# Kernel optimization log

Hardware: AMD Instinct MI355X
Metric: run time of the kernel (lower is better)

Reference implementation:

```python
import jax, jax.numpy as jnp
import numpy as np

E = 1024   # embed_dim
H = 16     # num_heads
D = E // H # head dim = 64
NUM_BUCKETS = 32
MAX_DISTANCE = 128


def _relative_position_bucket(rel, num_buckets=NUM_BUCKETS, max_distance=MAX_DISTANCE):
    # T5-style bucketing (bidirectional): sign half + log-spaced far buckets.
    nb = num_buckets // 2
    buckets = (rel > 0).astype(jnp.int32) * nb
    rel = jnp.abs(rel)
    max_exact = nb // 2
    is_small = rel < max_exact
    # clamp to >=1 before log to avoid -inf on the masked-out branch
    rel_f = jnp.maximum(rel, 1).astype(jnp.float32)
    large = max_exact + (
        jnp.log(rel_f / max_exact) / np.log(max_distance / max_exact) * (nb - max_exact)
    ).astype(jnp.int32)
    large = jnp.minimum(large, nb - 1)
    return buckets + jnp.where(is_small, rel, large)


def setup_inputs() -> dict:
    key = jax.random.key(0)
    ks = jax.random.split(key, 6)
    B, S, K = 2, 2048, 2048
    w = 0.02
    return {
        "hidden_states": jax.random.normal(ks[0], (B, S, E), jnp.float32),
        "key_value_states": jax.random.normal(ks[1], (B, K, E), jnp.float32),
        "Wq": jax.random.normal(ks[2], (E, E), jnp.float32) * w,
        "Wkv": jax.random.normal(ks[3], (E, 2 * E), jnp.float32) * w,
        "Wo": jax.random.normal(ks[4], (E, E), jnp.float32) * w,
        "rel_bias": jax.random.normal(ks[5], (NUM_BUCKETS, H), jnp.float32) * w,
    }


def reference(hidden_states, key_value_states, Wq, Wkv, Wo, rel_bias):
    B, S, _ = hidden_states.shape
    K = key_value_states.shape[1]
    # projections (no bias, no 1/sqrt(d) scaling — T5 style)
    q = (hidden_states @ Wq).reshape(B, S, H, D).transpose(0, 2, 1, 3)      # [B,H,S,D]
    kv = (key_value_states @ Wkv).reshape(B, K, 2, H, D)
    k = kv[:, :, 0].transpose(0, 2, 1, 3)                                   # [B,H,K,D]
    v = kv[:, :, 1].transpose(0, 2, 1, 3)                                   # [B,H,K,D]
    scores = jnp.einsum('bhsd,bhkd->bhsk', q, k)                            # [B,H,S,K]
    # relative position bias
    rel = jnp.arange(K)[None, :] - jnp.arange(S)[:, None]                   # [S,K]
    buckets = _relative_position_bucket(rel)                                # [S,K]
    bias = rel_bias[buckets].transpose(2, 0, 1)[None]                       # [1,H,S,K]
    scores = scores + bias
    attn = jax.nn.softmax(scores.astype(jnp.float32), axis=-1).astype(scores.dtype)
    out = jnp.einsum('bhsk,bhkd->bshd', attn, v).reshape(B, S, E)
    return out @ Wo
```

## Files before the change

kernel.cpp:

```cpp
#include <hip/hip_runtime.h>
#include <hip/hip_bf16.h>
#include <math.h>

typedef __hip_bfloat16 bf16;
typedef __bf16 bf16x4 __attribute__((ext_vector_type(4)));
typedef __bf16 bf16x8 __attribute__((ext_vector_type(8)));
typedef float f32x4 __attribute__((ext_vector_type(4)));
typedef float f32x16 __attribute__((ext_vector_type(16)));
typedef unsigned short us4 __attribute__((ext_vector_type(4)));

#define LOG2E 1.44269504088896340736f

#if defined(__has_builtin)
#if __has_builtin(__builtin_amdgcn_exp2f)
#define EXP2(x) __builtin_amdgcn_exp2f(x)
#else
#define EXP2(x) exp2f(x)
#endif
#else
#define EXP2(x) exp2f(x)
#endif


__device__ inline __bf16 f2b(float f) {
  __hip_bfloat16 h = __float2bfloat16(f);
  return *reinterpret_cast<__bf16*>(&h);
}
__device__ inline unsigned short b2u(float f) {
  __hip_bfloat16 h = __float2bfloat16(f);
  return *reinterpret_cast<unsigned short*>(&h);
}
__device__ inline unsigned short b2u_fast(float f) {
  union { float f; unsigned u; } v;
  v.f = f;
  return (unsigned short)((v.u + 0x8000u) >> 16);
}
__device__ inline bf16x8 ld16(const bf16* p) {
  bf16x4 lo = *(const bf16x4*)p;
  bf16x4 hi = *(const bf16x4*)(p + 4);
  return __builtin_shufflevector(lo, hi, 0, 1, 2, 3, 4, 5, 6, 7);
}
__device__ inline void st16(bf16* p, uint4 v) {
  *(uint2*)p = make_uint2(v.x, v.y);
  *(uint2*)(p + 4) = make_uint2(v.z, v.w);
}
__device__ inline us4 shfl32_us4(us4 v) {
  uint2 u = *(uint2*)&v;
  u.x = __shfl_xor(u.x, 32);
  u.y = __shfl_xor(u.y, 32);
  return *(us4*)&u;
}
__device__ inline bf16x8 mk8(us4 lo, us4 hi) {
  bf16x4 l = *(bf16x4*)&lo;
  bf16x4 h = *(bf16x4*)&hi;
  return __builtin_shufflevector(l, h, 0, 1, 2, 3, 4, 5, 6, 7);
}
__device__ inline void async16(const bf16* g, bf16* l) {
  __builtin_amdgcn_global_load_lds(
      (const __attribute__((address_space(1))) unsigned int*)g,
      (__attribute__((address_space(3))) unsigned int*)l, 16, 0, 0);
}

__global__ void cast2_k(const float* __restrict__ a, const float* __restrict__ b,
                        bf16* __restrict__ oa, bf16* __restrict__ ob) {
  int gid = blockIdx.x * 256 + threadIdx.x;
  const float* in = (gid < 524288) ? a : b;
  bf16* out = (gid < 524288) ? oa : ob;
  int i = (gid & 524287) * 8;
  float4 a0 = *(const float4*)(in + i);
  float4 a1 = *(const float4*)(in + i + 4);
  bf16x8 v;
  v[0] = f2b(a0.x); v[1] = f2b(a0.y); v[2] = f2b(a0.z); v[3] = f2b(a0.w);
  v[4] = f2b(a1.x); v[5] = f2b(a1.y); v[6] = f2b(a1.z); v[7] = f2b(a1.w);
  *(bf16x8*)(out + i) = v;
}

__global__ void prep_k(const float* __restrict__ Wq, const float* __restrict__ Wkv,
                       const float* __restrict__ Wo, const float* __restrict__ rel_bias,
                       bf16* __restrict__ WqT, bf16* __restrict__ WkvT,
                       bf16* __restrict__ WoT, float* __restrict__ lut) {
  __shared__ float tile[32][33];
  int z = blockIdx.z;
  int tx = threadIdx.x, ty = threadIdx.y;
  if (z == 3) {
    if (blockIdx.y != 0 || blockIdx.x >= 16) return;
    int r = blockIdx.x * 256 + ty * 32 + tx;
    int rel = r - 2048;
    int bkt = rel > 0 ? 16 : 0;
    int ar = rel < 0 ? -rel : rel;
    int idx;
    if (ar < 8) {
      idx = bkt + ar;
    } else {
      double t = log((double)ar / 8.0) / log(16.0) * 8.0;
      int lg = 8 + (int)t;
      if (lg > 15) lg = 15;
      idx = bkt + lg;
    }
    for (int h = 0; h < 16; ++h)
      lut[h * 4096 + r] = rel_bias[idx * 16 + h] * LOG2E;
    return;
  }
  const float* in = z == 0 ? Wq : (z == 1 ? Wkv : Wo);
  bf16* out = z == 0 ? WqT : (z == 1 ? WkvT : WoT);
  int cols = z == 1 ? 2048 : 1024;
  int c0 = blockIdx.x * 32;
  if (c0 >= cols) return;
  int r0 = blockIdx.y * 32;
  for (int i = ty; i < 32; i += 8)
    tile[i][tx] = in[(size_t)(r0 + i) * cols + c0 + tx];
  __syncthreads();
  for (int i = ty; i < 32; i += 8)
    out[(size_t)(c0 + i) * 1024 + r0 + tx] = __float2bfloat16(tile[tx][i]);
}

__global__ __launch_bounds__(256) void gemm_qkv_k(const bf16* __restrict__ hbf,
                                                  const bf16* __restrict__ kbf,
                                                  const bf16* __restrict__ WqT,
                                                  const bf16* __restrict__ WkvT,
                                                  bf16* __restrict__ Qb,
                                                  bf16* __restrict__ Kb,
                                                  bf16* __restrict__ Vt) {
  __shared__ __align__(16) bf16 As[128 * 32];
  __shared__ __align__(16) bf16 Bs[128 * 32];
  const int tid = threadIdx.x;
  const int lane = tid & 63;
  const int w = tid >> 6;
  const int wm = (w >> 1) * 64;
  const int wn = (w & 1) * 64;
  const int l15 = lane & 15;
  const int quad = lane >> 4;
  const int srow = lane >> 2;
  const int skg = lane & 3;

  const bool isQ = blockIdx.y < 8;
  const bf16* A = isQ ? hbf : kbf;
  const bf16* Bt = isQ ? WqT : WkvT;
  const int n0 = (isQ ? blockIdx.y : blockIdx.y - 8) * 128;
  const int m0 = blockIdx.x * 128;
  const bool isV = (!isQ) && (n0 >= 1024);

  f32x4 acc[4][4];
#pragma unroll
  for (int i = 0; i < 4; ++i)
#pragma unroll
    for (int j = 0; j < 4; ++j) acc[i][j] = (f32x4){0.f, 0.f, 0.f, 0.f};

  for (int k0 = 0; k0 < 1024; k0 += 32) {
    __syncthreads();
#pragma unroll
    for (int rep = 0; rep < 2; ++rep) {
      int seg = w * 2 + rep;
      async16(A + (size_t)(m0 + seg * 16 + srow) * 1024 + k0 + skg * 8, As + seg * 512);
      async16(Bt + (size_t)(n0 + seg * 16 + srow) * 1024 + k0 + skg * 8, Bs + seg * 512);
    }
    __syncthreads();
    bf16x8 af[4], bfr[4];
#pragma unroll
    for (int i = 0; i < 4; ++i)
      af[i] = *(const bf16x8*)(As + (wm + i * 16 + l15) * 32 + quad * 8);
#pragma unroll
    for (int j = 0; j < 4; ++j)
      bfr[j] = *(const bf16x8*)(Bs + (wn + j * 16 + l15) * 32 + quad * 8);
    if (isV) {
#pragma unroll
      for (int i = 0; i < 4; ++i)
#pragma unroll
        for (int j = 0; j < 4; ++j)
          acc[i][j] = __builtin_amdgcn_mfma_f32_16x16x32_bf16(af[i], bfr[j], acc[i][j], 0, 0, 0);
    } else {
#pragma unroll
      for (int i = 0; i < 4; ++i)
#pragma unroll
        for (int j = 0; j < 4; ++j)
          acc[i][j] = __builtin_amdgcn_mfma_f32_16x16x32_bf16(bfr[j], af[i], acc[i][j], 0, 0, 0);
    }
  }

  if (isV) {
#pragma unroll
    for (int i = 0; i < 4; ++i) {
      int gmb = m0 + wm + i * 16 + quad * 4;
      int b = gmb >> 11, kp = gmb & 2047;
#pragma unroll
      for (int j = 0; j < 4; ++j) {
        int gn = n0 + wn + j * 16 + l15;
        int h = (gn >> 6) & 15, d = gn & 63;
        us4 pk;
#pragma unroll
        for (int r = 0; r < 4; ++r) pk[r] = b2u(acc[i][j][r]);
        *(us4*)(Vt + ((((size_t)b * 16 + h) * 64 + d) << 11) + kp) = pk;
      }
    }
    return;
  }
  const float scale = isQ ? LOG2E : 1.0f;
  bf16* dst = isQ ? Qb : Kb;
#pragma unroll
  for (int i = 0; i < 4; ++i) {
    int gm = m0 + wm + i * 16 + l15;
    int b = gm >> 11, s = gm & 2047;
#pragma unroll
    for (int j = 0; j < 4; ++j) {
      int gn = n0 + wn + j * 16 + quad * 4;
      int h = (gn >> 6) & 15, d0 = gn & 63;
      us4 pk;
#pragma unroll
      for (int r = 0; r < 4; ++r) pk[r] = b2u(acc[i][j][r] * scale);
      *(us4*)(dst + ((((size_t)b * 16 + h) * 2048 + s) << 6) + d0) = pk;
    }
  }
}

__global__ __launch_bounds__(256) void gemm_o_k(const bf16* __restrict__ A,
                                                const bf16* __restrict__ Bt,
                                                float* __restrict__ C0) {
  __shared__ __align__(16) bf16 As[128 * 32];
  __shared__ __align__(16) bf16 Bs[64 * 32];
  const int tid = threadIdx.x;
  const int lane = tid & 63;
  const int w = tid >> 6;
  const int wm = w * 32;
  const int m0 = blockIdx.x * 128;
  const int n0 = blockIdx.y * 64;
  const int l15 = lane & 15;
  const int quad = lane >> 4;
  const int srow = lane >> 2;
  const int skg = lane & 3;

  f32x4 acc[2][4];
#pragma unroll
  for (int i = 0; i < 2; ++i)
#pragma unroll
    for (int j = 0; j < 4; ++j) acc[i][j] = (f32x4){0.f, 0.f, 0.f, 0.f};

  for (int k0 = 0; k0 < 1024; k0 += 32) {
    __syncthreads();
#pragma unroll
    for (int rep = 0; rep < 2; ++rep) {
      int seg = w * 2 + rep;
      async16(A + (size_t)(m0 + seg * 16 + srow) * 1024 + k0 + skg * 8, As + seg * 512);
    }
    async16(Bt + (size_t)(n0 + w * 16 + srow) * 1024 + k0 + skg * 8, Bs + w * 512);
    __syncthreads();
    bf16x8 af[2], bfr[4];
#pragma unroll
    for (int i = 0; i < 2; ++i)
      af[i] = *(const bf16x8*)(As + (wm + i * 16 + l15) * 32 + quad * 8);
#pragma unroll
    for (int j = 0; j < 4; ++j)
      bfr[j] = *(const bf16x8*)(Bs + (j * 16 + l15) * 32 + quad * 8);
#pragma unroll
    for (int i = 0; i < 2; ++i)
#pragma unroll
      for (int j = 0; j < 4; ++j)
        acc[i][j] = __builtin_amdgcn_mfma_f32_16x16x32_bf16(bfr[j], af[i], acc[i][j], 0, 0, 0);
  }
#pragma unroll
  for (int i = 0; i < 2; ++i) {
    int gm = m0 + wm + i * 16 + l15;
#pragma unroll
    for (int j = 0; j < 4; ++j) {
      int gn = n0 + j * 16 + quad * 4;
      *(f32x4*)(C0 + (size_t)gm * 1024 + gn) = acc[i][j];
    }
  }
}

#define STK 68
#define SVK 136
#define KS_OFF 8704
#define VS_OFF 43520
__global__ __launch_bounds__(512, 2) void attn_k(const bf16* __restrict__ Qb,
                                                 const bf16* __restrict__ Kb,
                                                 const bf16* __restrict__ Vt,
                                                 const float* __restrict__ lut,
                                                 bf16* __restrict__ Ob) {
  __shared__ __align__(16) char smem[78336];
  float* lbias = (float*)smem;
  bf16* Ksb = (bf16*)(smem + KS_OFF);
  bf16* Vsb = (bf16*)(smem + VS_OFF);

  const int tid = threadIdx.x;
  const int lane = tid & 63;
  const int w = tid >> 6;
  const int wq = w & 3;
  const int kg = w >> 2;
  const int t256 = tid & 255;
  const int q31 = lane & 31;
  const int half = lane >> 5;

  bf16* Ks = Ksb + kg * (128 * STK);
  bf16* Vs = Vsb + kg * (64 * SVK);

  const int qt = blockIdx.x;
  const int bh = blockIdx.y;
  const int h = bh & 15, b = bh >> 4;
  const int qb = qt * 128;

  const int gbase = h * 4096 + 1921 - qb;
  for (int t = tid; t < 2175; t += 512) lbias[t] = lut[gbase + t];

  const size_t base = (size_t)bh * 2048 * 64;
  const size_t vbase = (size_t)bh * 64 * 2048;
  const int qg = qb + wq * 32 + q31;

  bf16x8 qf[4];
#pragma unroll
  for (int c = 0; c < 4; ++c)
    qf[c] = *(const bf16x8*)(Qb + base + (size_t)qg * 64 + c * 16 + half * 8);

  f32x16 oacc[2];
#pragma unroll
  for (int dj = 0; dj < 2; ++dj)
#pragma unroll
    for (int r = 0; r < 16; ++r) oacc[dj][r] = 0.f;
  float l_run = 0.f;

  const int kt0 = kg * 128;

  uint4 kr[4], vr[4];
#pragma unroll
  for (int rep = 0; rep < 4; ++rep) {
    int slot = t256 + rep * 256;
    kr[rep] = *(const uint4*)(Kb + base + (size_t)(kt0 + (slot >> 3)) * 64 + (slot & 7) * 8);
    vr[rep] = *(const uint4*)(Vt + vbase + (size_t)(slot >> 4) * 2048 + kt0 + (slot & 15) * 8);
  }

  for (int it = 0; it < 8; ++it) {
    const int kt = it * 256 + kt0;
    __syncthreads();
#pragma unroll
    for (int rep = 0; rep < 4; ++rep) {
      int slot = t256 + rep * 256;
      st16(Ks + (slot >> 3) * STK + (slot & 7) * 8, kr[rep]);
      st16(Vs + (slot >> 4) * SVK + (slot & 15) * 8, vr[rep]);
    }
    __syncthreads();
    if (it < 7) {
      const int nkt = kt + 256;
#pragma unroll
      for (int rep = 0; rep < 4; ++rep) {
        int slot = t256 + rep * 256;
        kr[rep] = *(const uint4*)(Kb + base + (size_t)(nkt + (slot >> 3)) * 64 + (slot & 7) * 8);
        vr[rep] = *(const uint4*)(Vt + vbase + (size_t)(slot >> 4) * 2048 + nkt + (slot & 15) * 8);
      }
    }

    const int xbase = kt + 127 + 4 * half - wq * 32 - q31;
#pragma unroll
    for (int mt = 0; mt < 4; ++mt) {
      f32x16 sacc;
#pragma unroll
      for (int a2 = 0; a2 < 4; ++a2)
#pragma unroll
        for (int rr = 0; rr < 4; ++rr)
          sacc[4 * a2 + rr] = lbias[xbase + mt * 32 + 8 * a2 + rr];
#pragma unroll
      for (int c = 0; c < 4; ++c) {
        bf16x8 kf = ld16(Ks + (mt * 32 + q31) * STK + c * 16 + half * 8);
        sacc = __builtin_amdgcn_mfma_f32_32x32x16_bf16(kf, qf[c], sacc, 0, 0, 0);
      }

      us4 ownq[4];
      f32x4 sv = (f32x4){0.f, 0.f, 0.f, 0.f};
#pragma unroll
      for (int a = 0; a < 4; ++a) {
        us4 pk;
#pragma unroll
        for (int rr = 0; rr < 4; ++rr) {
          float p = EXP2(sacc[4 * a + rr]);
          sv[rr] += p;
          pk[rr] = b2u_fast(p);
        }
        ownq[a] = pk;
      }
      l_run += (sv[0] + sv[1]) + (sv[2] + sv[3]);

      us4 rcv0 = shfl32_us4(half ? ownq[0] : ownq[1]);
      us4 rcv1 = shfl32_us4(half ? ownq[2] : ownq[3]);

#pragma unroll
      for (int p = 0; p < 2; ++p) {
        us4 rc = p ? rcv1 : rcv0;
        bf16x8 pfc = half ? mk8(rc, ownq[2 * p + 1]) : mk8(ownq[2 * p], rc);
#pragma unroll
        for (int dj = 0; dj < 2; ++dj) {
          bf16x8 vf = ld16(Vs + (dj * 32 + q31) * SVK + (mt * 2 + p) * 16 + half * 8);
          oacc[dj] = __builtin_amdgcn_mfma_f32_32x32x16_bf16(vf, pfc, oacc[dj], 0, 0, 0);
        }
      }
    }
  }

  l_run += __shfl_xor(l_run, 32);

  __syncthreads();
  float* mbuf = (float*)smem;
  if (kg) {
    float* p = mbuf + ((size_t)(wq * 64 + lane)) * 35;
    p[0] = l_run;
#pragma unroll
    for (int dj = 0; dj < 2; ++dj)
#pragma unroll
      for (int r = 0; r < 16; ++r) p[1 + dj * 16 + r] = oacc[dj][r];
  }
  __syncthreads();
  if (kg) return;

  const float* p = mbuf + ((size_t)(wq * 64 + lane)) * 35;
  float inv = 1.0f / (l_run + p[0]);

#pragma unroll
  for (int dj = 0; dj < 2; ++dj)
#pragma unroll
    for (int g = 0; g < 4; ++g) {
      us4 pk;
#pragma unroll
      for (int rr = 0; rr < 4; ++rr)
        pk[rr] = b2u((oacc[dj][4 * g + rr] + p[1 + dj * 16 + 4 * g + rr]) * inv);
      int d0 = dj * 32 + 8 * g + 4 * half;
      *(us4*)(Ob + ((size_t)(b * 2048 + qg)) * 1024 + h * 64 + d0) = pk;
    }
}

extern "C" void kernel_launch(void* const* d_in, const int* in_sizes, int n_in,
                              void* d_out, int out_size, void* d_ws, size_t ws_size,
                              hipStream_t stream) {
  const float* hidden = (const float*)d_in[0];
  const float* kvs    = (const float*)d_in[1];
  const float* Wq     = (const float*)d_in[2];
  const float* Wkv    = (const float*)d_in[3];
  const float* Wo     = (const float*)d_in[4];
  const float* relb   = (const float*)d_in[5];
  float* out = (float*)d_out;

  char* ws = (char*)d_ws;
  bf16* WqT  = (bf16*)(ws + (size_t)0);
  bf16* WkvT = (bf16*)(ws + ((size_t)2 << 20));
  bf16* WoT  = (bf16*)(ws + ((size_t)6 << 20));
  bf16* Ob   = (bf16*)(ws + ((size_t)8 << 20));
  bf16* hbf  = Ob;
  bf16* Qb   = (bf16*)(ws + ((size_t)16 << 20));
  bf16* Kb   = (bf16*)(ws + ((size_t)24 << 20));
  bf16* Vt   = (bf16*)(ws + ((size_t)32 << 20));
  float* LUT = (float*)(ws + ((size_t)40 << 20));
  bf16* kbf  = (bf16*)d_out;

  prep_k<<<dim3(64, 32, 4), dim3(32, 8), 0, stream>>>(Wq, Wkv, Wo, relb, WqT, WkvT, WoT, LUT);
  cast2_k<<<4096, 256, 0, stream>>>(hidden, kvs, hbf, kbf);
  gemm_qkv_k<<<dim3(32, 24), 256, 0, stream>>>(hbf, kbf, WqT, WkvT, Qb, Kb, Vt);
  attn_k<<<dim3(16, 32), 512, 0, stream>>>(Qb, Kb, Vt, LUT, Ob);
  gemm_o_k<<<dim3(32, 16), 256, 0, stream>>>(Ob, WoT, out);
}
```

Measured before the change: 226.9 us.

## Remap attention blocks so each XCD owns whole heads; drop K/V register prefetch

The attention grid becomes 1D. Block ids are remapped so all 16 query tiles of a given batch-head land on the same XCD (blocks are assigned to XCDs round-robin), which should let that XCD's L2 reuse the K/V tiles. The register-staged prefetch of the next K/V tile is also removed: each tile is now loaded and stored to shared memory in the same iteration. This cuts register pressure and may raise occupancy, but load latency is no longer hidden behind compute.

After: 218.8 us (median of 2 runs). 3.6% less time.

```diff
diff --git a/kernel.cpp b/kernel.cpp
--- a/kernel.cpp
+++ b/kernel.cpp
@@ -293,8 +293,11 @@
   bf16* Ks = Ksb + kg * (128 * STK);
   bf16* Vs = Vsb + kg * (64 * SVK);
 
-  const int qt = blockIdx.x;
-  const int bh = blockIdx.y;
+  const int wg = blockIdx.x;
+  const int xcd = wg & 7;
+  const int slot = wg >> 3;
+  const int bh = xcd * 4 + (slot >> 4);
+  const int qt = slot & 15;
   const int h = bh & 15, b = bh >> 4;
   const int qb = qt * 128;
 
@@ -319,33 +322,25 @@
 
   const int kt0 = kg * 128;
 
-  uint4 kr[4], vr[4];
-#pragma unroll
-  for (int rep = 0; rep < 4; ++rep) {
-    int slot = t256 + rep * 256;
-    kr[rep] = *(const uint4*)(Kb + base + (size_t)(kt0 + (slot >> 3)) * 64 + (slot & 7) * 8);
-    vr[rep] = *(const uint4*)(Vt + vbase + (size_t)(slot >> 4) * 2048 + kt0 + (slot & 15) * 8);
-  }
-
   for (int it = 0; it < 8; ++it) {
     const int kt = it * 256 + kt0;
     __syncthreads();
-#pragma unroll
-    for (int rep = 0; rep < 4; ++rep) {
-      int slot = t256 + rep * 256;
-      st16(Ks + (slot >> 3) * STK + (slot & 7) * 8, kr[rep]);
-      st16(Vs + (slot >> 4) * SVK + (slot & 15) * 8, vr[rep]);
-    }
-    __syncthreads();
-    if (it < 7) {
-      const int nkt = kt + 256;
+    {
+      uint4 kr[4], vr[4];
 #pragma unroll
       for (int rep = 0; rep < 4; ++rep) {
-        int slot = t256 + rep * 256;
-        kr[rep] = *(const uint4*)(Kb + base + (size_t)(nkt + (slot >> 3)) * 64 + (slot & 7) * 8);
-        vr[rep] = *(const uint4*)(Vt + vbase + (size_t)(slot >> 4) * 2048 + nkt + (slot & 15) * 8);
-      }
-    }
+        int slot2 = t256 + rep * 256;
+        kr[rep] = *(const uint4*)(Kb + base + (size_t)(kt + (slot2 >> 3)) * 64 + (slot2 & 7) * 8);
+        vr[rep] = *(const uint4*)(Vt + vbase + (size_t)(slot2 >> 4) * 2048 + kt + (slot2 & 15) * 8);
+      }
+#pragma unroll
+      for (int rep = 0; rep < 4; ++rep) {
+        int slot2 = t256 + rep * 256;
+        st16(Ks + (slot2 >> 3) * STK + (slot2 & 7) * 8, kr[rep]);
+        st16(Vs + (slot2 >> 4) * SVK + (slot2 & 15) * 8, vr[rep]);
+      }
+    }
+    __syncthreads();
 
     const int xbase = kt + 127 + 4 * half - wq * 32 - q31;
 #pragma unroll
@@ -450,6 +445,6 @@
   prep_k<<<dim3(64, 32, 4), dim3(32, 8), 0, stream>>>(Wq, Wkv, Wo, relb, WqT, WkvT, WoT, LUT);
   cast2_k<<<4096, 256, 0, stream>>>(hidden, kvs, hbf, kbf);
   gemm_qkv_k<<<dim3(32, 24), 256, 0, stream>>>(hbf, kbf, WqT, WkvT, Qb, Kb, Vt);
-  attn_k<<<dim3(16, 32), 512, 0, stream>>>(Qb, Kb, Vt, LUT, Ob);
+  attn_k<<<dim3(512), 512, 0, stream>>>(Qb, Kb, Vt, LUT, Ob);
   gemm_o_k<<<dim3(32, 16), 256, 0, stream>>>(Ob, WoT, out);
 }
```
